# Performance work log

Hardware: AMD Instinct MI355X
Metric: run time of the kernel (lower is better)

The kernel has to match this reference:

```python
import jax, jax.numpy as jnp
import numpy as np

B, S, H = 2, 2048, 2048
NH, G = 32, 8
D = H // NH          # head dim = 64
R = NH // G          # q heads per kv group = 4
SCALE = 1.0 / np.sqrt(D)


def setup_inputs() -> dict:
    key = jax.random.key(0)
    ks = jax.random.split(key, 9)
    s = 0.02
    return {
        "x": jax.random.normal(ks[0], (B, S, H), jnp.float32),
        "Wq": jax.random.normal(ks[1], (H, H), jnp.float32) * s,
        "bq": jnp.zeros((H,), jnp.float32),
        "Wk": jax.random.normal(ks[2], (H, G * D), jnp.float32) * s,
        "bk": jnp.zeros((G * D,), jnp.float32),
        "Wv": jax.random.normal(ks[3], (H, G * D), jnp.float32) * s,
        "bv": jnp.zeros((G * D,), jnp.float32),
        "Wo": jax.random.normal(ks[4], (H, H), jnp.float32) * s,
        "bo": jnp.zeros((H,), jnp.float32),
    }


def reference(x, Wq, bq, Wk, bk, Wv, bv, Wo, bo):
    # projections
    q = x @ Wq + bq                                  # [B,S,H]
    k = x @ Wk + bk                                  # [B,S,G*D]
    v = x @ Wv + bv                                  # [B,S,G*D]
    # split heads: q -> [B,G,R,S,D]; k,v -> [B,G,S,D]
    q = q.reshape(B, S, G, R, D).transpose(0, 2, 3, 1, 4)
    k = k.reshape(B, S, G, D).transpose(0, 2, 1, 3)
    v = v.reshape(B, S, G, D).transpose(0, 2, 1, 3)
    # grouped attention without materializing expanded KV
    scores = jnp.einsum('bgrqd,bgkd->bgrqk', q, k) * SCALE   # [B,G,R,S,S]
    weights = jax.nn.softmax(scores, axis=-1)
    out = jnp.einsum('bgrqk,bgkd->bgrqd', weights, v)        # [B,G,R,S,D]
    # merge heads: head index = g*R + r (matches torch expand/reshape order)
    out = out.transpose(0, 3, 1, 2, 4).reshape(B, S, H)
    return out @ Wo + bo
```

## Files before the change

kernel.cpp:

```cpp
#include <hip/hip_runtime.h>
#include <stdint.h>

#define S_LEN 2048
#define HDIM  2048
#define BATCH 2
#define NKV   8
#define GD    512
#define MROWS 4096
#define NQKV  3072

typedef __attribute__((ext_vector_type(8))) __bf16 bf16x8;
typedef __attribute__((ext_vector_type(4))) float f32x4;
typedef __attribute__((ext_vector_type(16))) float f32x16;
typedef unsigned short u16;

__device__ __forceinline__ u16 bfc(float f) {
  union { __bf16 b; u16 u; } v; v.b = (__bf16)f; return v.u;
}
__device__ __forceinline__ int cvtpk(float lo, float hi) {
  int r; asm("v_cvt_pk_bf16_f32 %0, %1, %2" : "=v"(r) : "v"(lo), "v"(hi)); return r;
}

__device__ __forceinline__ void glds16(const void* g, void* lds) {
  __builtin_amdgcn_global_load_lds((const __attribute__((address_space(1))) void*)g,
                                   (__attribute__((address_space(3))) void*)lds, 16, 0, 0);
}

__global__ __launch_bounds__(256) void cvt_f32_bf16_kernel(const float* __restrict__ x,
                                                           u16* __restrict__ y, int n4) {
  int i = blockIdx.x * 256 + threadIdx.x;
  if (i >= n4) return;
  const float4 v = ((const float4*)x)[i];
  ushort4 o;
  o.x = bfc(v.x); o.y = bfc(v.y); o.z = bfc(v.z); o.w = bfc(v.w);
  ((ushort4*)y)[i] = o;
}

__global__ __launch_bounds__(256) void concat_bias_kernel(const float* __restrict__ bq,
                                                          const float* __restrict__ bk,
                                                          const float* __restrict__ bv,
                                                          float* __restrict__ o) {
  int i = blockIdx.x * 256 + threadIdx.x;
  if (i < HDIM) o[i] = bq[i];
  else if (i < HDIM + GD) o[i] = bk[i - HDIM];
  else if (i < NQKV) o[i] = bv[i - HDIM - GD];
}

__global__ __launch_bounds__(256) void transpose_f32_bf16(const float* __restrict__ W,
                                                          u16* __restrict__ Wt,
                                                          int Rr, int Cc) {
  __shared__ float t[32][33];
  int bx = blockIdx.x * 32;
  int by = blockIdx.y * 32;
  int tx = threadIdx.x & 31, ty = threadIdx.x >> 5;
#pragma unroll
  for (int i = 0; i < 4; ++i)
    t[ty + i * 8][tx] = W[(size_t)(by + ty + i * 8) * Cc + bx + tx];
  __syncthreads();
#pragma unroll
  for (int i = 0; i < 4; ++i)
    Wt[(size_t)(bx + ty + i * 8) * Rr + by + tx] = bfc(t[tx][ty + i * 8]);
}

__global__ __launch_bounds__(256) void transpose_v_kernel(const u16* __restrict__ QKV,
                                                          u16* __restrict__ Vt) {
  __shared__ u16 t[32][33];
  int b = blockIdx.z;
  const u16* Vb = QKV + (size_t)b * S_LEN * NQKV + HDIM + GD;
  u16* Vtb = Vt + (size_t)b * GD * S_LEN;
  int bx = blockIdx.x * 32;
  int by = blockIdx.y * 32;
  int tx = threadIdx.x & 31, ty = threadIdx.x >> 5;
#pragma unroll
  for (int i = 0; i < 4; ++i)
    t[ty + i * 8][tx] = Vb[(size_t)(by + ty + i * 8) * NQKV + bx + tx];
  __syncthreads();
#pragma unroll
  for (int i = 0; i < 4; ++i)
    Vtb[(size_t)(bx + ty + i * 8) * S_LEN + by + tx] = t[tx][ty + i * 8];
}

__global__ __launch_bounds__(256) void gemm_bf16(const u16* __restrict__ A,
                                                 const u16* __restrict__ Bt,
                                                 const float* __restrict__ bias,
                                                 void* __restrict__ C,
                                                 int M, int N, int K,
                                                 float alphaA, float alphaB, int qlim,
                                                 int obf) {
  __shared__ __attribute__((aligned(16))) u16 As[128 * 32];
  __shared__ __attribute__((aligned(16))) u16 Bs[128 * 32];
  const int tid = threadIdx.x, lane = tid & 63, wv = tid >> 6;
  const int wr = wv >> 1, wc = wv & 1;
  const int r16 = lane & 15, kg = lane >> 4;

  const int nwg = gridDim.x * gridDim.y;
  const int orig = blockIdx.y * gridDim.x + blockIdx.x;
  const int qq = nwg >> 3, rr = nwg & 7;
  const int xcd = orig & 7, loc = orig >> 3;
  const int swz = (xcd < rr ? xcd * (qq + 1) : rr * (qq + 1) + (xcd - rr) * qq) + loc;
  const int m0 = (swz / gridDim.x) * 128, n0 = (swz % gridDim.x) * 128;
  const float alpha = (n0 < qlim) ? alphaA : alphaB;

  f32x4 acc[4][4];
#pragma unroll
  for (int m = 0; m < 4; ++m)
#pragma unroll
    for (int n = 0; n < 4; ++n) acc[m][n] = (f32x4)0.0f;

  auto stage = [&](int k0) {
#pragma unroll
    for (int i = 0; i < 2; ++i) {
      int chunk = i * 256 + wv * 64 + lane;
      int row = chunk >> 2, cc = chunk & 3;
      glds16(A + (size_t)(m0 + row) * K + k0 + cc * 8, &As[(i * 256 + wv * 64) * 8]);
    }
#pragma unroll
    for (int i = 0; i < 2; ++i) {
      int chunk = i * 256 + wv * 64 + lane;
      int row = chunk >> 2, cc = chunk & 3;
      glds16(Bt + (size_t)(n0 + row) * K + k0 + cc * 8, &Bs[(i * 256 + wv * 64) * 8]);
    }
  };

  stage(0);
  const int nk = K / 32;
  for (int kt = 0; kt < nk; ++kt) {
    asm volatile("s_waitcnt vmcnt(0)" ::: "memory");
    __syncthreads();
    bf16x8 af[4], bfr[4];
#pragma unroll
    for (int m = 0; m < 4; ++m)
      af[m] = *(const bf16x8*)&As[(wr * 64 + m * 16 + r16) * 32 + kg * 8];
#pragma unroll
    for (int n = 0; n < 4; ++n)
      bfr[n] = *(const bf16x8*)&Bs[(wc * 64 + n * 16 + r16) * 32 + kg * 8];
    __syncthreads();
    if (kt + 1 < nk) stage((kt + 1) * 32);
#pragma unroll
    for (int m = 0; m < 4; ++m)
#pragma unroll
      for (int n = 0; n < 4; ++n)
        acc[m][n] = __builtin_amdgcn_mfma_f32_16x16x32_bf16(af[m], bfr[n], acc[m][n], 0, 0, 0);
  }

#pragma unroll
  for (int m = 0; m < 4; ++m) {
    int row = m0 + wr * 64 + m * 16 + kg * 4;
#pragma unroll
    for (int n = 0; n < 4; ++n) {
      int col = n0 + wc * 64 + n * 16 + r16;
      float bb = bias ? bias[col] : 0.0f;
#pragma unroll
      for (int i = 0; i < 4; ++i) {
        float val = (acc[m][n][i] + bb) * alpha;
        if (obf) ((u16*)C)[(size_t)(row + i) * N + col] = bfc(val);
        else     ((float*)C)[(size_t)(row + i) * N + col] = val;
      }
    }
  }
}

__global__ __launch_bounds__(256, 4) void gqa_attn_kernel(const u16* __restrict__ qkv,
                                                          const u16* __restrict__ vT,
                                                          u16* __restrict__ att) {
  __shared__ __attribute__((aligned(16))) u16 Ks[2][64 * 64];
  __shared__ __attribute__((aligned(16))) u16 Vs[2][64 * 64];

  const int bid = blockIdx.x;
  const int qt = bid & 15;
  const int h = (bid >> 4) & 31;
  const int b = bid >> 9;
  const int g = h >> 2;
  const int tid = threadIdx.x, lane = tid & 63, wv = tid >> 6;
  const int q31 = lane & 31, hi = lane >> 5;
  const int qbase = qt * 128 + wv * 32;

  const u16* qrow = qkv + (size_t)(b * S_LEN + qbase + q31) * NQKV + h * 64;
  bf16x8 qf[4];
#pragma unroll
  for (int d = 0; d < 4; ++d)
    qf[d] = *(const bf16x8*)(qrow + d * 16 + hi * 8);

  union { u16 w[8]; bf16x8 v; } uo;
#pragma unroll
  for (int i = 0; i < 8; ++i) uo.w[i] = 0x3F80;
  const bf16x8 onesf = uo.v;

  const u16* kbase = qkv + (size_t)(b * S_LEN) * NQKV + HDIM + g * 64;
  const u16* vbase = vT + (size_t)((b * NKV + g) * 64) * S_LEN;

  auto stageK = [&](int kk0, int buf) {
#pragma unroll
    for (int i = 0; i < 2; ++i) {
      int chunk = i * 256 + wv * 64 + lane;
      int row = chunk >> 3, cc = chunk & 7;
      int cs = cc ^ (row & 7);
      glds16(kbase + (size_t)(kk0 + row) * NQKV + cs * 8, &Ks[buf][(i * 256 + wv * 64) * 8]);
      glds16(vbase + (size_t)row * S_LEN + kk0 + cs * 8, &Vs[buf][(i * 256 + wv * 64) * 8]);
    }
  };

  f32x16 o0 = (f32x16)0.0f, o1 = (f32x16)0.0f, ol = (f32x16)0.0f;

  stageK(0, 0);
  int cur = 0;
  const int sw = q31 & 7;
  for (int t = 0; t < S_LEN / 64; ++t) {
    asm volatile("s_waitcnt vmcnt(0)" ::: "memory");
    __syncthreads();
    if (t + 1 < S_LEN / 64) stageK((t + 1) * 64, cur ^ 1);

    f32x16 p0 = (f32x16)0.0f, p1 = (f32x16)0.0f;
    __builtin_amdgcn_s_setprio(1);
#pragma unroll
    for (int d = 0; d < 4; ++d) {
      int ch = ((d * 2 + hi) ^ sw) * 8;
      bf16x8 kf0 = *(const bf16x8*)&Ks[cur][q31 * 64 + ch];
      bf16x8 kf1 = *(const bf16x8*)&Ks[cur][(32 + q31) * 64 + ch];
      p0 = __builtin_amdgcn_mfma_f32_32x32x16_bf16(kf0, qf[d], p0, 0, 0, 0);
      p1 = __builtin_amdgcn_mfma_f32_32x32x16_bf16(kf1, qf[d], p1, 0, 0, 0);
    }
    __builtin_amdgcn_s_setprio(0);

#pragma unroll
    for (int r = 0; r < 16; ++r) {
      p0[r] = exp2f(p0[r]);
      p1[r] = exp2f(p1[r]);
    }

    bf16x8 pa[4];
#pragma unroll
    for (int kk = 0; kk < 2; ++kk) {
      int w0 = cvtpk(p0[kk * 8 + 0], p0[kk * 8 + 1]);
      int w1 = cvtpk(p0[kk * 8 + 2], p0[kk * 8 + 3]);
      int w2 = cvtpk(p0[kk * 8 + 4], p0[kk * 8 + 5]);
      int w3 = cvtpk(p0[kk * 8 + 6], p0[kk * 8 + 7]);
      auto s0 = __builtin_amdgcn_permlane32_swap(w0, w2, false, false);
      auto s1 = __builtin_amdgcn_permlane32_swap(w1, w3, false, false);
      union { int w[4]; bf16x8 v; } u;
      u.w[0] = s0[0]; u.w[1] = s1[0]; u.w[2] = s0[1]; u.w[3] = s1[1];
      pa[kk] = u.v;
    }
#pragma unroll
    for (int kk = 0; kk < 2; ++kk) {
      int w0 = cvtpk(p1[kk * 8 + 0], p1[kk * 8 + 1]);
      int w1 = cvtpk(p1[kk * 8 + 2], p1[kk * 8 + 3]);
      int w2 = cvtpk(p1[kk * 8 + 4], p1[kk * 8 + 5]);
      int w3 = cvtpk(p1[kk * 8 + 6], p1[kk * 8 + 7]);
      auto s0 = __builtin_amdgcn_permlane32_swap(w0, w2, false, false);
      auto s1 = __builtin_amdgcn_permlane32_swap(w1, w3, false, false);
      union { int w[4]; bf16x8 v; } u;
      u.w[0] = s0[0]; u.w[1] = s1[0]; u.w[2] = s0[1]; u.w[3] = s1[1];
      pa[2 + kk] = u.v;
    }

    __builtin_amdgcn_s_setprio(1);
#pragma unroll
    for (int ks = 0; ks < 4; ++ks) {
      int ch = (((ks * 2 + hi)) ^ sw) * 8;
      bf16x8 vf0 = *(const bf16x8*)&Vs[cur][q31 * 64 + ch];
      bf16x8 vf1 = *(const bf16x8*)&Vs[cur][(32 + q31) * 64 + ch];
      o0 = __builtin_amdgcn_mfma_f32_32x32x16_bf16(pa[ks], vf0, o0, 0, 0, 0);
      o1 = __builtin_amdgcn_mfma_f32_32x32x16_bf16(pa[ks], vf1, o1, 0, 0, 0);
      ol = __builtin_amdgcn_mfma_f32_32x32x16_bf16(pa[ks], onesf, ol, 0, 0, 0);
    }
    __builtin_amdgcn_s_setprio(0);
    cur ^= 1;
  }

  u16* obase = att + (size_t)(b * S_LEN + qbase) * HDIM + h * 64 + q31;
#pragma unroll
  for (int r = 0; r < 16; ++r) {
    int qq = (r & 3) + 8 * (r >> 2) + 4 * hi;
    float inv = 1.0f / ol[r];
    obase[(size_t)qq * HDIM]      = bfc(o0[r] * inv);
    obase[(size_t)qq * HDIM + 32] = bfc(o1[r] * inv);
  }
}

extern "C" void kernel_launch(void* const* d_in, const int* in_sizes, int n_in,
                              void* d_out, int out_size, void* d_ws, size_t ws_size,
                              hipStream_t stream) {
  const float* x  = (const float*)d_in[0];
  const float* Wq = (const float*)d_in[1];
  const float* bq = (const float*)d_in[2];
  const float* Wk = (const float*)d_in[3];
  const float* bk = (const float*)d_in[4];
  const float* Wv = (const float*)d_in[5];
  const float* bv = (const float*)d_in[6];
  const float* Wo = (const float*)d_in[7];
  const float* bo = (const float*)d_in[8];
  float* out = (float*)d_out;

  char* p = (char*)d_ws;
  u16* xb    = (u16*)p; p += (size_t)MROWS * HDIM * 2;
  u16* wqkvT = (u16*)p; p += (size_t)NQKV * HDIM * 2;
  u16* woT   = (u16*)p; p += (size_t)HDIM * HDIM * 2;
  float* bqkv = (float*)p; p += (size_t)NQKV * 4;
  u16* qkv   = (u16*)p; p += (size_t)MROWS * NQKV * 2;
  u16* vtb   = (u16*)p; p += (size_t)MROWS * GD * 2;
  u16* attb  = (u16*)p; p += (size_t)MROWS * HDIM * 2;

  const float aQ = 0.18033688011112042f;

  cvt_f32_bf16_kernel<<<(MROWS * HDIM / 4 + 255) / 256, 256, 0, stream>>>(x, xb, MROWS * HDIM / 4);
  transpose_f32_bf16<<<dim3(HDIM / 32, HDIM / 32), 256, 0, stream>>>(Wq, wqkvT, HDIM, HDIM);
  transpose_f32_bf16<<<dim3(GD / 32, HDIM / 32), 256, 0, stream>>>(Wk, wqkvT + (size_t)HDIM * HDIM, HDIM, GD);
  transpose_f32_bf16<<<dim3(GD / 32, HDIM / 32), 256, 0, stream>>>(Wv, wqkvT + (size_t)(HDIM + GD) * HDIM, HDIM, GD);
  transpose_f32_bf16<<<dim3(HDIM / 32, HDIM / 32), 256, 0, stream>>>(Wo, woT, HDIM, HDIM);
  concat_bias_kernel<<<(NQKV + 255) / 256, 256, 0, stream>>>(bq, bk, bv, bqkv);
  gemm_bf16<<<dim3(NQKV / 128, MROWS / 128), 256, 0, stream>>>(xb, wqkvT, bqkv, qkv,
                                                               MROWS, NQKV, HDIM, aQ, 1.0f, HDIM, 1);
  transpose_v_kernel<<<dim3(GD / 32, S_LEN / 32, BATCH), 256, 0, stream>>>(qkv, vtb);
  gqa_attn_kernel<<<BATCH * 32 * 16, 256, 0, stream>>>(qkv, vtb, attb);
  gemm_bf16<<<dim3(HDIM / 128, MROWS / 128), 256, 0, stream>>>(attb, woT, bo, out,
                                                               MROWS, HDIM, HDIM, 1.0f, 1.0f, HDIM, 0);
}
```

Measured before the change: 243.4 us.

## Process two 32-row query tiles per wave in attention to reuse K/V fragments

```diff
diff --git a/kernel.cpp b/kernel.cpp
--- a/kernel.cpp
+++ b/kernel.cpp
@@ -160,26 +160,29 @@
   }
 }
 
-__global__ __launch_bounds__(256, 4) void gqa_attn_kernel(const u16* __restrict__ qkv,
+__global__ __launch_bounds__(256, 2) void gqa_attn_kernel(const u16* __restrict__ qkv,
                                                           const u16* __restrict__ vT,
                                                           u16* __restrict__ att) {
   __shared__ __attribute__((aligned(16))) u16 Ks[2][64 * 64];
   __shared__ __attribute__((aligned(16))) u16 Vs[2][64 * 64];
 
   const int bid = blockIdx.x;
-  const int qt = bid & 15;
-  const int h = (bid >> 4) & 31;
-  const int b = bid >> 9;
+  const int qt = bid & 7;
+  const int h = (bid >> 3) & 31;
+  const int b = bid >> 8;
   const int g = h >> 2;
   const int tid = threadIdx.x, lane = tid & 63, wv = tid >> 6;
   const int q31 = lane & 31, hi = lane >> 5;
-  const int qbase = qt * 128 + wv * 32;
-
-  const u16* qrow = qkv + (size_t)(b * S_LEN + qbase + q31) * NQKV + h * 64;
-  bf16x8 qf[4];
-#pragma unroll
-  for (int d = 0; d < 4; ++d)
-    qf[d] = *(const bf16x8*)(qrow + d * 16 + hi * 8);
+  const int qbase = qt * 256 + wv * 64;
+
+  const u16* qrowA = qkv + (size_t)(b * S_LEN + qbase + q31) * NQKV + h * 64;
+  const u16* qrowB = qrowA + (size_t)32 * NQKV;
+  bf16x8 qfA[4], qfB[4];
+#pragma unroll
+  for (int d = 0; d < 4; ++d) {
+    qfA[d] = *(const bf16x8*)(qrowA + d * 16 + hi * 8);
+    qfB[d] = *(const bf16x8*)(qrowB + d * 16 + hi * 8);
+  }
 
   union { u16 w[8]; bf16x8 v; } uo;
 #pragma unroll
@@ -200,7 +203,8 @@
     }
   };
 
-  f32x16 o0 = (f32x16)0.0f, o1 = (f32x16)0.0f, ol = (f32x16)0.0f;
+  f32x16 o0A = (f32x16)0.0f, o1A = (f32x16)0.0f, olA = (f32x16)0.0f;
+  f32x16 o0B = (f32x16)0.0f, o1B = (f32x16)0.0f, olB = (f32x16)0.0f;
 
   stageK(0, 0);
   int cur = 0;
@@ -210,48 +214,73 @@
     __syncthreads();
     if (t + 1 < S_LEN / 64) stageK((t + 1) * 64, cur ^ 1);
 
-    f32x16 p0 = (f32x16)0.0f, p1 = (f32x16)0.0f;
+    f32x16 pA0 = (f32x16)0.0f, pA1 = (f32x16)0.0f;
+    f32x16 pB0 = (f32x16)0.0f, pB1 = (f32x16)0.0f;
     __builtin_amdgcn_s_setprio(1);
 #pragma unroll
     for (int d = 0; d < 4; ++d) {
       int ch = ((d * 2 + hi) ^ sw) * 8;
       bf16x8 kf0 = *(const bf16x8*)&Ks[cur][q31 * 64 + ch];
       bf16x8 kf1 = *(const bf16x8*)&Ks[cur][(32 + q31) * 64 + ch];
-      p0 = __builtin_amdgcn_mfma_f32_32x32x16_bf16(kf0, qf[d], p0, 0, 0, 0);
-      p1 = __builtin_amdgcn_mfma_f32_32x32x16_bf16(kf1, qf[d], p1, 0, 0, 0);
+      pA0 = __builtin_amdgcn_mfma_f32_32x32x16_bf16(kf0, qfA[d], pA0, 0, 0, 0);
+      pA1 = __builtin_amdgcn_mfma_f32_32x32x16_bf16(kf1, qfA[d], pA1, 0, 0, 0);
+      pB0 = __builtin_amdgcn_mfma_f32_32x32x16_bf16(kf0, qfB[d], pB0, 0, 0, 0);
+      pB1 = __builtin_amdgcn_mfma_f32_32x32x16_bf16(kf1, qfB[d], pB1, 0, 0, 0);
     }
     __builtin_amdgcn_s_setprio(0);
 
 #pragma unroll
-    for (int r = 0; r < 16; ++r) {
-      p0[r] = exp2f(p0[r]);
-      p1[r] = exp2f(p1[r]);
-    }
-
-    bf16x8 pa[4];
+    for (int r = 0; r < 16; ++r) { pA0[r] = exp2f(pA0[r]); pA1[r] = exp2f(pA1[r]); }
+    bf16x8 paA[4], paB[4];
 #pragma unroll
     for (int kk = 0; kk < 2; ++kk) {
-      int w0 = cvtpk(p0[kk * 8 + 0], p0[kk * 8 + 1]);
-      int w1 = cvtpk(p0[kk * 8 + 2], p0[kk * 8 + 3]);
-      int w2 = cvtpk(p0[kk * 8 + 4], p0[kk * 8 + 5]);
-      int w3 = cvtpk(p0[kk * 8 + 6], p0[kk * 8 + 7]);
+      int w0 = cvtpk(pA0[kk * 8 + 0], pA0[kk * 8 + 1]);
+      int w1 = cvtpk(pA0[kk * 8 + 2], pA0[kk * 8 + 3]);
+      int w2 = cvtpk(pA0[kk * 8 + 4], pA0[kk * 8 + 5]);
+      int w3 = cvtpk(pA0[kk * 8 + 6], pA0[kk * 8 + 7]);
       auto s0 = __builtin_amdgcn_permlane32_swap(w0, w2, false, false);
       auto s1 = __builtin_amdgcn_permlane32_swap(w1, w3, false, false);
       union { int w[4]; bf16x8 v; } u;
       u.w[0] = s0[0]; u.w[1] = s1[0]; u.w[2] = s0[1]; u.w[3] = s1[1];
-      pa[kk] = u.v;
+      paA[kk] = u.v;
     }
 #pragma unroll
     for (int kk = 0; kk < 2; ++kk) {
-      int w0 = cvtpk(p1[kk * 8 + 0], p1[kk * 8 + 1]);
-      int w1 = cvtpk(p1[kk * 8 + 2], p1[kk * 8 + 3]);
-      int w2 = cvtpk(p1[kk * 8 + 4], p1[kk * 8 + 5]);
-      int w3 = cvtpk(p1[kk * 8 + 6], p1[kk * 8 + 7]);
+      int w0 = cvtpk(pA1[kk * 8 + 0], pA1[kk * 8 + 1]);
+      int w1 = cvtpk(pA1[kk * 8 + 2], pA1[kk * 8 + 3]);
+      int w2 = cvtpk(pA1[kk * 8 + 4], pA1[kk * 8 + 5]);
+      int w3 = cvtpk(pA1[kk * 8 + 6], pA1[kk * 8 + 7]);
       auto s0 = __builtin_amdgcn_permlane32_swap(w0, w2, false, false);
       auto s1 = __builtin_amdgcn_permlane32_swap(w1, w3, false, false);
       union { int w[4]; bf16x8 v; } u;
       u.w[0] = s0[0]; u.w[1] = s1[0]; u.w[2] = s0[1]; u.w[3] = s1[1];
-      pa[2 + kk] = u.v;
+      paA[2 + kk] = u.v;
+    }
+#pragma unroll
+    for (int r = 0; r < 16; ++r) { pB0[r] = exp2f(pB0[r]); pB1[r] = exp2f(pB1[r]); }
+#pragma unroll
+    for (int kk = 0; kk < 2; ++kk) {
+      int w0 = cvtpk(pB0[kk * 8 + 0], pB0[kk * 8 + 1]);
+      int w1 = cvtpk(pB0[kk * 8 + 2], pB0[kk * 8 + 3]);
+      int w2 = cvtpk(pB0[kk * 8 + 4], pB0[kk * 8 + 5]);
+      int w3 = cvtpk(pB0[kk * 8 + 6], pB0[kk * 8 + 7]);
+      auto s0 = __builtin_amdgcn_permlane32_swap(w0, w2, false, false);
+      auto s1 = __builtin_amdgcn_permlane32_swap(w1, w3, false, false);
+      union { int w[4]; bf16x8 v; } u;
+      u.w[0] = s0[0]; u.w[1] = s1[0]; u.w[2] = s0[1]; u.w[3] = s1[1];
+      paB[kk] = u.v;
+    }
+#pragma unroll
+    for (int kk = 0; kk < 2; ++kk) {
+      int w0 = cvtpk(pB1[kk * 8 + 0], pB1[kk * 8 + 1]);
+      int w1 = cvtpk(pB1[kk * 8 + 2], pB1[kk * 8 + 3]);
+      int w2 = cvtpk(pB1[kk * 8 + 4], pB1[kk * 8 + 5]);
+      int w3 = cvtpk(pB1[kk * 8 + 6], pB1[kk * 8 + 7]);
+      auto s0 = __builtin_amdgcn_permlane32_swap(w0, w2, false, false);
+      auto s1 = __builtin_amdgcn_permlane32_swap(w1, w3, false, false);
+      union { int w[4]; bf16x8 v; } u;
+      u.w[0] = s0[0]; u.w[1] = s1[0]; u.w[2] = s0[1]; u.w[3] = s1[1];
+      paB[2 + kk] = u.v;
     }
 
     __builtin_amdgcn_s_setprio(1);
@@ -260,9 +289,12 @@
       int ch = (((ks * 2 + hi)) ^ sw) * 8;
       bf16x8 vf0 = *(const bf16x8*)&Vs[cur][q31 * 64 + ch];
       bf16x8 vf1 = *(const bf16x8*)&Vs[cur][(32 + q31) * 64 + ch];
-      o0 = __builtin_amdgcn_mfma_f32_32x32x16_bf16(pa[ks], vf0, o0, 0, 0, 0);
-      o1 = __builtin_amdgcn_mfma_f32_32x32x16_bf16(pa[ks], vf1, o1, 0, 0, 0);
-      ol = __builtin_amdgcn_mfma_f32_32x32x16_bf16(pa[ks], onesf, ol, 0, 0, 0);
+      o0A = __builtin_amdgcn_mfma_f32_32x32x16_bf16(paA[ks], vf0, o0A, 0, 0, 0);
+      o1A = __builtin_amdgcn_mfma_f32_32x32x16_bf16(paA[ks], vf1, o1A, 0, 0, 0);
+      o0B = __builtin_amdgcn_mfma_f32_32x32x16_bf16(paB[ks], vf0, o0B, 0, 0, 0);
+      o1B = __builtin_amdgcn_mfma_f32_32x32x16_bf16(paB[ks], vf1, o1B, 0, 0, 0);
+      olA = __builtin_amdgcn_mfma_f32_32x32x16_bf16(paA[ks], onesf, olA, 0, 0, 0);
+      olB = __builtin_amdgcn_mfma_f32_32x32x16_bf16(paB[ks], onesf, olB, 0, 0, 0);
     }
     __builtin_amdgcn_s_setprio(0);
     cur ^= 1;
@@ -272,9 +304,12 @@
 #pragma unroll
   for (int r = 0; r < 16; ++r) {
     int qq = (r & 3) + 8 * (r >> 2) + 4 * hi;
-    float inv = 1.0f / ol[r];
-    obase[(size_t)qq * HDIM]      = bfc(o0[r] * inv);
-    obase[(size_t)qq * HDIM + 32] = bfc(o1[r] * inv);
+    float invA = 1.0f / olA[r];
+    float invB = 1.0f / olB[r];
+    obase[(size_t)qq * HDIM]             = bfc(o0A[r] * invA);
+    obase[(size_t)qq * HDIM + 32]        = bfc(o1A[r] * invA);
+    obase[(size_t)(qq + 32) * HDIM]      = bfc(o0B[r] * invB);
+    obase[(size_t)(qq + 32) * HDIM + 32] = bfc(o1B[r] * invB);
   }
 }
 
@@ -312,7 +347,7 @@
   gemm_bf16<<<dim3(NQKV / 128, MROWS / 128), 256, 0, stream>>>(xb, wqkvT, bqkv, qkv,
                                                                MROWS, NQKV, HDIM, aQ, 1.0f, HDIM, 1);
   transpose_v_kernel<<<dim3(GD / 32, S_LEN / 32, BATCH), 256, 0, stream>>>(qkv, vtb);
-  gqa_attn_kernel<<<BATCH * 32 * 16, 256, 0, stream>>>(qkv, vtb, attb);
+  gqa_attn_kernel<<<BATCH * 32 * 8, 256, 0, stream>>>(qkv, vtb, attb);
   gemm_bf16<<<dim3(HDIM / 128, MROWS / 128), 256, 0, stream>>>(attb, woT, bo, out,
                                                                MROWS, HDIM, HDIM, 1.0f, 1.0f, HDIM, 0);
 }
```

After: 243.0 us. Within noise of the previous version (-0.1%).
